# Performance work log

Hardware: AMD Instinct MI355X
Metric: run time of the kernel (lower is better)

Reference implementation:

```python
import jax, jax.numpy as jnp
import numpy as np

B, T, U, V = 4, 300, 80, 1024
DE, DD, INNER = 320, 320, 512


def setup_inputs() -> dict:
    key = jax.random.key(0)
    ks = jax.random.split(key, 6)
    enc_state = jax.random.normal(ks[0], (B, T, DE), jnp.float32)
    dec_state = jax.random.normal(ks[1], (B, U + 1, DD), jnp.float32)
    Wf = jax.random.normal(ks[2], (INNER, DE + DD), jnp.float32) / np.float32(np.sqrt(DE + DD))
    bf = jnp.zeros((INNER,), jnp.float32)
    Wp = jax.random.normal(ks[3], (V, INNER), jnp.float32) / np.float32(np.sqrt(INNER))
    bp = jnp.zeros((V,), jnp.float32)
    targets = jax.random.randint(ks[4], (B, U), 1, V).astype(jnp.int32)  # labels avoid blank=0
    inputs_length = jnp.full((B,), T, jnp.int32)
    targets_length = jnp.full((B,), U, jnp.int32)
    return {"enc_state": enc_state, "dec_state": dec_state, "Wf": Wf, "bf": bf,
            "Wp": Wp, "bp": bp, "targets": targets,
            "inputs_length": inputs_length, "targets_length": targets_length}


def joint_logits(enc, dec, Wf, bf, Wp, bp):
    # Linear over concat([enc, dec]) == Linear(enc) + Linear(dec): avoids materializing the concat.
    de = enc.shape[-1]
    Wf_e, Wf_d = Wf[:, :de], Wf[:, de:]
    enc_p = jnp.einsum('btd,id->bti', enc, Wf_e)   # [B,T,inner]
    dec_p = jnp.einsum('bud,id->bui', dec, Wf_d)   # [B,U1,inner]
    h = jnp.tanh(enc_p[:, :, None, :] + dec_p[:, None, :, :] + bf)  # [B,T,U1,inner]
    return jnp.einsum('btui,vi->btuv', h, Wp) + bp  # [B,T,U1,V]


def rnnt_loss(log_probs, targets, t_len, u_len):
    # log_probs: [B,T,U1,V], blank index 0.
    lp_blank = log_probs[..., 0]  # [B,T,U1]
    lp_emit = jnp.take_along_axis(log_probs[:, :, :-1, :], targets[:, None, :, None], axis=3)[..., 0]  # [B,T,U]
    # row0: alpha[0,u] = sum_{k<u} emit[0,k]
    row0 = jnp.pad(jnp.cumsum(lp_emit[:, 0, :], axis=-1), ((0, 0), (1, 0)))  # [B,U1]

    def outer(alpha_prev, xs):
        blank_prev, emit_cur = xs  # [B,U1], [B,U]
        first = alpha_prev[:, 0] + blank_prev[:, 0]  # [B]

        def inner(c, x):
            a_plus_b, e = x  # [B],[B]
            c2 = jnp.logaddexp(a_plus_b, c + e)
            return c2, c2
        xs_in = ((alpha_prev[:, 1:] + blank_prev[:, 1:]).T, emit_cur.T)  # [U,B]
        _, rest = jax.lax.scan(inner, first, xs_in)  # [U,B]
        row = jnp.concatenate([first[None, :], rest], axis=0).T  # [B,U1]
        return row, row

    xs = (jnp.swapaxes(lp_blank[:, :-1, :], 0, 1), jnp.swapaxes(lp_emit[:, 1:, :], 0, 1))
    _, rows = jax.lax.scan(outer, row0, xs)  # [T-1,B,U1]
    alpha = jnp.concatenate([row0[None], rows], axis=0)  # [T,B,U1]
    bidx = jnp.arange(alpha.shape[1])
    ll = alpha[t_len - 1, bidx, u_len] + lp_blank[bidx, t_len - 1, u_len]
    return -jnp.mean(ll)


def reference(enc_state, dec_state, Wf, bf, Wp, bp, targets, inputs_length, targets_length):
    logits = joint_logits(enc_state, dec_state, Wf, bf, Wp, bp).astype(jnp.float32)
    log_probs = jax.nn.log_softmax(logits, axis=-1)
    return rnnt_loss(log_probs, targets, inputs_length, targets_length)
```

## Files before the change

### kernel.cpp

```cpp
#include <hip/hip_runtime.h>

#define B_DIM 4
#define T_DIM 300
#define U_DIM 80
#define UP1   81
#define V_DIM 1024
#define NINNER 512
#define NROWS (B_DIM * T_DIM * UP1)
#define EP_ROWS (B_DIM * T_DIM)
#define DP_ROWS (B_DIM * UP1)
#define NDIAG_B 380
#define NDIAG_E 379
#define DSTRIDE 82
#define WF_PART 163840
#define LOG2E 1.44269504088896341f
#define LN2   0.69314718055994531f
#define NEGF  -1e30f

typedef float f32x4 __attribute__((ext_vector_type(4)));
typedef short short8 __attribute__((ext_vector_type(8)));
typedef short short4v __attribute__((ext_vector_type(4)));
typedef __bf16 bf16x8 __attribute__((ext_vector_type(8)));

static __device__ __forceinline__ short f2bf(float f) {
  return (short)__builtin_bit_cast(unsigned short, (__bf16)f);
}
static __device__ __forceinline__ float bf2f(short s) {
  unsigned int u = ((unsigned int)(unsigned short)s) << 16;
  return __builtin_bit_cast(float, u);
}
static __device__ __forceinline__ float tanh_fast(float x) {
  float e = __builtin_amdgcn_exp2f(x * 2.88539008177792681f);
  return 1.0f - 2.0f * __builtin_amdgcn_rcpf(e + 1.0f);
}
static __device__ __forceinline__ float lse2_2(float a, float b) {
  float mx = fmaxf(a, b), mn = fminf(a, b);
  return mx + __builtin_amdgcn_logf(1.0f + __builtin_amdgcn_exp2f(mn - mx));
}
static __device__ __forceinline__ float ror1f(float x) {
  int r = __builtin_amdgcn_update_dpp(0, __builtin_bit_cast(int, x),
                                      0x13C , 0xF, 0xF, true);
  return __builtin_bit_cast(float, r);
}
static __device__ __forceinline__ float readlanef(float x, int l) {
  return __builtin_bit_cast(float,
      __builtin_amdgcn_readlane(__builtin_bit_cast(int, x), l));
}

__global__ __launch_bounds__(256) void fill_kernel(float* __restrict__ dst, int n4) {
  int i = blockIdx.x * 256 + threadIdx.x;
  if (i < n4) ((f32x4*)dst)[i] = (f32x4){NEGF, NEGF, NEGF, NEGF};
}

__global__ __launch_bounds__(256) void cvt_kernel(
    const float* __restrict__ Wf, const float* __restrict__ Wp,
    short* __restrict__ WfB, short* __restrict__ WpB) {
  int idx = blockIdx.x * 256 + threadIdx.x;
  const int nf = (512 * 640) / 4;
  const int np = (V_DIM * NINNER) / 4;
  if (idx < nf) {
    float4 v = ((const float4*)Wf)[idx];
    int flat = idx * 4;
    int c = flat / 640;
    int kc = flat - c * 640;
    int part = (kc >= 320);
    int k0 = kc - (part ? 320 : 0);
    int dest = (part ? WF_PART : 0)
             + ((c >> 4) * 10 + (k0 >> 5)) * 512
             + (((k0 >> 3) & 3) * 16 + (c & 15)) * 8 + (k0 & 7);
    short4v o;
    o[0] = f2bf(v.x); o[1] = f2bf(v.y); o[2] = f2bf(v.z); o[3] = f2bf(v.w);
    *(short4v*)(WfB + dest) = o;
  } else if (idx < nf + np) {
    int j = idx - nf;
    float4 v = ((const float4*)Wp)[j];
    int flat = j * 4;
    int c = flat >> 9;
    int k0 = flat & 511;
    int dest = ((c >> 4) * 16 + (k0 >> 5)) * 512
             + (((k0 >> 3) & 3) * 16 + (c & 15)) * 8 + (k0 & 7);
    short4v o;
    o[0] = f2bf(v.x); o[1] = f2bf(v.y); o[2] = f2bf(v.z); o[3] = f2bf(v.w);
    *(short4v*)(WpB + dest) = o;
  }
}

#define EP_BLOCKS 19
__global__ __launch_bounds__(256) void proj_kernel(
    const float* __restrict__ enc, const float* __restrict__ dec,
    const short* __restrict__ WfB, const float* __restrict__ bfv,
    short* __restrict__ epB, short* __restrict__ dpB) {
  const int half = blockIdx.x & 1;
  const int ob = blockIdx.x >> 1;
  const bool is_dp = (ob >= EP_BLOCKS);
  const int row0 = (is_dp ? ob - EP_BLOCKS : ob) * 64;
  const int nrows = is_dp ? DP_ROWS : EP_ROWS;
  const float* __restrict__ src = is_dp ? dec : enc;
  const short* __restrict__ bb = WfB + (is_dp ? WF_PART : 0);
  short* __restrict__ out = is_dp ? dpB : epB;

  __shared__ short As[64 * 320];
  const int tid = threadIdx.x;

  #pragma unroll
  for (int it = 0; it < 10; ++it) {
    int chunk = it * 256 + tid;
    int m = chunk / 40;
    int c = chunk - m * 40;
    int r = row0 + m;
    short8 hv;
    #pragma unroll
    for (int j = 0; j < 8; ++j) hv[j] = 0;
    if (r < nrows) {
      const float* p = src + (size_t)r * 320 + c * 8;
      float4 a0 = *(const float4*)p;
      float4 a1 = *(const float4*)(p + 4);
      hv[0] = f2bf(a0.x); hv[1] = f2bf(a0.y); hv[2] = f2bf(a0.z); hv[3] = f2bf(a0.w);
      hv[4] = f2bf(a1.x); hv[5] = f2bf(a1.y); hv[6] = f2bf(a1.z); hv[7] = f2bf(a1.w);
    }
    int off = (m * 640 + c * 16) ^ ((m & 7) << 4);
    *(short8*)((char*)As + off) = hv;
  }
  __syncthreads();

  const int lane = tid & 63, wid = tid >> 6;
  const int lr = lane & 15, g = lane >> 4;

  int lin[4], xm[4];
  #pragma unroll
  for (int mf = 0; mf < 4; ++mf) {
    int row = mf * 16 + lr;
    lin[mf] = row * 640 + g * 16;
    xm[mf] = (row & 7) << 4;
  }

  const int n0 = half * 256 + wid * 64;
  const short* bptr[4];
  float bfc[4];
  #pragma unroll
  for (int nf2 = 0; nf2 < 4; ++nf2) {
    bptr[nf2] = bb + (n0 / 16 + nf2) * 5120 + lane * 8;
    bfc[nf2] = is_dp ? bfv[n0 + nf2 * 16 + lr] : 0.f;
  }
  f32x4 acc[4][4];
  #pragma unroll
  for (int mf = 0; mf < 4; ++mf)
    #pragma unroll
    for (int nf2 = 0; nf2 < 4; ++nf2)
      acc[mf][nf2] = (f32x4){0.f, 0.f, 0.f, 0.f};

  #pragma unroll 2
  for (int kk = 0; kk < 10; ++kk) {
    bf16x8 av[4], bv[4];
    #pragma unroll
    for (int mf = 0; mf < 4; ++mf) {
      int off = (lin[mf] + (kk << 6)) ^ xm[mf];
      av[mf] = __builtin_bit_cast(bf16x8, *(const short8*)((const char*)As + off));
    }
    #pragma unroll
    for (int nf2 = 0; nf2 < 4; ++nf2)
      bv[nf2] = __builtin_bit_cast(bf16x8, *(const short8*)(bptr[nf2] + kk * 512));
    #pragma unroll
    for (int mf = 0; mf < 4; ++mf)
      #pragma unroll
      for (int nf2 = 0; nf2 < 4; ++nf2)
        acc[mf][nf2] = __builtin_amdgcn_mfma_f32_16x16x32_bf16(av[mf], bv[nf2], acc[mf][nf2], 0, 0, 0);
  }
  #pragma unroll
  for (int mf = 0; mf < 4; ++mf)
    #pragma unroll
    for (int nf2 = 0; nf2 < 4; ++nf2)
      #pragma unroll
      for (int rr = 0; rr < 4; ++rr) {
        int rowl = mf * 16 + g * 4 + rr;
        int grow = row0 + rowl;
        if (grow < nrows) {
          int col = n0 + nf2 * 16 + lr;
          out[(size_t)grow * NINNER + col] = f2bf(acc[mf][nf2][rr] + bfc[nf2]);
        }
      }
}

#define JROWS 64
__global__ __launch_bounds__(512) void joint_kernel(
    const short* __restrict__ epB, const short* __restrict__ dpB,
    const short* __restrict__ WpB, const float* __restrict__ bp,
    const int* __restrict__ tgt,
    float* __restrict__ lpb_p, float* __restrict__ lpe_p) {
  extern __shared__ char hbuf[];
  __shared__ int ep_off[JROWS], dp_off[JROWS], bld_off[JROWS], eld_off[JROWS], tgt_s[JROWS];
  __shared__ float l0_s[JROWS], lt_s[JROWS];
  __shared__ float ws_s[8][JROWS];

  const int tid = threadIdx.x;
  const int row0 = blockIdx.x * JROWS;

  if (tid < JROWS) {
    int gr = row0 + tid;
    if (gr < NROWS) {
      int b = gr / (T_DIM * UP1);
      int rem = gr - b * (T_DIM * UP1);
      int t = rem / UP1;
      int u = rem - t * UP1;
      ep_off[tid] = (b * T_DIM + t) * NINNER;
      dp_off[tid] = (b * UP1 + u) * NINNER;
      bld_off[tid] = (b * NDIAG_B + (t + u)) * DSTRIDE + 1 + u;
      eld_off[tid] = (u < U_DIM) ? ((b * NDIAG_E + (t + u)) * DSTRIDE + 2 + u) : -1;
      tgt_s[tid] = (u < U_DIM) ? tgt[b * U_DIM + u] : 0;
    } else {
      ep_off[tid] = 0; dp_off[tid] = 0; bld_off[tid] = -1; eld_off[tid] = -1; tgt_s[tid] = 0;
    }
    l0_s[tid] = 0.f; lt_s[tid] = 0.f;
  }
  __syncthreads();

  #pragma unroll 2
  for (int it = 0; it < 8; ++it) {
    int chunk = it * 512 + tid;
    int m = chunk >> 6, c = chunk & 63;
    short8 hv;
    #pragma unroll
    for (int j = 0; j < 8; ++j) hv[j] = 0;
    if (bld_off[m] >= 0) {
      short8 ev = *(const short8*)(epB + ep_off[m] + c * 8);
      short8 dv = *(const short8*)(dpB + dp_off[m] + c * 8);
      #pragma unroll
      for (int j = 0; j < 8; ++j)
        hv[j] = f2bf(tanh_fast(bf2f(ev[j]) + bf2f(dv[j])));
    }
    int off = ((m << 10) + (c << 4)) ^ ((m & 7) << 4);
    *(short8*)(hbuf + off) = hv;
  }
  __syncthreads();

  const int lane = tid & 63, wid = tid >> 6;
  const int lr = lane & 15, g = lane >> 4;

  int lin[4], xm[4];
  #pragma unroll
  for (int mf = 0; mf < 4; ++mf) {
    int row = mf * 16 + lr;
    lin[mf] = (row << 10) + (g << 4);
    xm[mf] = (row & 7) << 4;
  }
  int tv[4][4];
  #pragma unroll
  for (int mf = 0; mf < 4; ++mf)
    #pragma unroll
    for (int rr = 0; rr < 4; ++rr)
      tv[mf][rr] = tgt_s[mf * 16 + g * 4 + rr];

  float rsum[4][4];
  #pragma unroll
  for (int mf = 0; mf < 4; ++mf)
    #pragma unroll
    for (int rr = 0; rr < 4; ++rr) rsum[mf][rr] = 0.f;

  #pragma unroll
  for (int sc = 0; sc < 2; ++sc) {
    const int n0 = wid * 128 + sc * 64;
    const short* bptr[4];
    float bpv[4];
    #pragma unroll
    for (int nf = 0; nf < 4; ++nf) {
      bptr[nf] = WpB + (n0 / 16 + nf) * 8192 + lane * 8;
      bpv[nf] = bp[n0 + nf * 16 + lr] * LOG2E;
    }
    f32x4 acc[4][4];
    #pragma unroll
    for (int mf = 0; mf < 4; ++mf)
      #pragma unroll
      for (int nf = 0; nf < 4; ++nf)
        acc[mf][nf] = (f32x4){0.f, 0.f, 0.f, 0.f};

    #pragma unroll 2
    for (int kk = 0; kk < 16; ++kk) {
      bf16x8 av[4], bv[4];
      #pragma unroll
      for (int mf = 0; mf < 4; ++mf) {
        int off = (lin[mf] + (kk << 6)) ^ xm[mf];
        av[mf] = __builtin_bit_cast(bf16x8, *(const short8*)(hbuf + off));
      }
      #pragma unroll
      for (int nf = 0; nf < 4; ++nf)
        bv[nf] = __builtin_bit_cast(bf16x8, *(const short8*)(bptr[nf] + kk * 512));
      __builtin_amdgcn_s_setprio(1);
      #pragma unroll
      for (int mf = 0; mf < 4; ++mf)
        #pragma unroll
        for (int nf = 0; nf < 4; ++nf)
          acc[mf][nf] = __builtin_amdgcn_mfma_f32_16x16x32_bf16(av[mf], bv[nf], acc[mf][nf], 0, 0, 0);
      __builtin_amdgcn_s_setprio(0);
    }
    #pragma unroll
    for (int mf = 0; mf < 4; ++mf)
      #pragma unroll
      for (int rr = 0; rr < 4; ++rr) {
        float x0 = __builtin_fmaf(acc[mf][0][rr], LOG2E, bpv[0]);
        float x1 = __builtin_fmaf(acc[mf][1][rr], LOG2E, bpv[1]);
        float x2 = __builtin_fmaf(acc[mf][2][rr], LOG2E, bpv[2]);
        float x3 = __builtin_fmaf(acc[mf][3][rr], LOG2E, bpv[3]);
        int rowl = mf * 16 + g * 4 + rr;
        if (wid == 0 && sc == 0 && lr == 0) l0_s[rowl] = x0;
        int dtv = tv[mf][rr] - n0;
        if (dtv >= 0 && dtv < 64 && (dtv & 15) == lr) {
          int nfi = dtv >> 4;
          lt_s[rowl] = (nfi == 0) ? x0 : (nfi == 1) ? x1 : (nfi == 2) ? x2 : x3;
        }
        rsum[mf][rr] += __builtin_amdgcn_exp2f(x0) + __builtin_amdgcn_exp2f(x1)
                      + __builtin_amdgcn_exp2f(x2) + __builtin_amdgcn_exp2f(x3);
      }
  }
  #pragma unroll
  for (int mf = 0; mf < 4; ++mf)
    #pragma unroll
    for (int rr = 0; rr < 4; ++rr) {
      float s_ = rsum[mf][rr];
      #pragma unroll
      for (int o = 1; o < 16; o <<= 1) s_ += __shfl_xor(s_, o);
      if (lr == 0) ws_s[wid][mf * 16 + g * 4 + rr] = s_;
    }
  __syncthreads();
  if (tid < JROWS) {
    int bo = bld_off[tid];
    if (bo >= 0) {
      float S = 0.f;
      #pragma unroll
      for (int w = 0; w < 8; ++w) S += ws_s[w][tid];
      float lse2v = __builtin_amdgcn_logf(S);
      lpb_p[bo] = l0_s[tid] - lse2v;
      int eo = eld_off[tid];
      if (eo >= 0) lpe_p[eo] = lt_s[tid] - lse2v;
    }
  }
}

#define ACH 8
#define NCH 48
__global__ __launch_bounds__(256) void alpha_kernel(
    const float* __restrict__ lpb_p, const float* __restrict__ lpe_p,
    const int* __restrict__ ilen, const int* __restrict__ ulen_,
    float* __restrict__ out) {
  __shared__ float lls[B_DIM];
  const int tid = threadIdx.x;
  const int b = tid >> 6;
  const int lane = tid & 63;
  const float NEG = NEGF;
  const int tl = ilen[b], ul = ulen_[b];
  const int dstar = tl - 1 + ul;

  const int u0 = lane;
  const int u1 = 64 + lane;
  const bool act1 = (u1 <= 80);
  const int uc1 = act1 ? u1 : 80;

  const float* pbb = lpb_p + (size_t)b * (NDIAG_B * DSTRIDE);
  const float* peb = lpe_p + (size_t)b * (NDIAG_E * DSTRIDE);

  float Ab0r[ACH], Ab0m[ACH], Ae0r[ACH], Ae0m[ACH];
  float Ab1r[ACH], Ab1m[ACH], Ae1r[ACH], Ae1m[ACH];
  float Bb0r[ACH], Bb0m[ACH], Be0r[ACH], Be0m[ACH];
  float Bb1r[ACH], Bb1m[ACH], Be1r[ACH], Be1m[ACH];

  #define ALOAD(P, c)                                                        \
    {                                                                        \
      _Pragma("unroll")                                                      \
      for (int j = 0; j < ACH; ++j) {                                        \
        int dd = (c) * ACH + j;                                              \
        int ddb = dd < NDIAG_B ? dd : NDIAG_B - 1;                           \
        int dde = dd < NDIAG_E ? dd : NDIAG_E - 1;                           \
        const float* rb_ = pbb + ddb * DSTRIDE + 1;                          \
        const float* re_ = peb + dde * DSTRIDE + 2;                          \
        P##b0r[j] = rb_[u0];                                                 \
        P##b0m[j] = rb_[u0 - 1];                                             \
        P##e0r[j] = re_[u0 - 1];                                             \
        P##e0m[j] = re_[u0 - 2];                                             \
        P##b1r[j] = rb_[uc1];                                                \
        P##b1m[j] = rb_[uc1 - 1];                                            \
        P##e1r[j] = re_[uc1 - 1];                                            \
        P##e1m[j] = re_[uc1 - 2];                                            \
      }                                                                      \
    }

  #define ACOMP(P, c)                                                        \
    {                                                                        \
      _Pragma("unroll")                                                      \
      for (int q = 0; q < ACH / 2; ++q) {                                    \
        const int j = 2 * q;                                                 \
        const int s1 = (c) * ACH + j + 1;                                    \
             \
        float a63 = readlanef(pa0, 63), a62 = readlanef(pa0, 62);            \
        float s0m1 = ror1f(pa0);                                             \
        float s0m2 = ror1f(s0m1);                                            \
        float s1m1r = ror1f(pa1);                                            \
        float s1m2r = ror1f(s1m1r);                                          \
        float s1m1 = (lane == 0) ? a63 : s1m1r;                              \
        float s1m2 = (lane == 0) ? a62 : ((lane == 1) ? a63 : s1m2r);        \
        float na0, na1;                                                      \
        {               \
          float b1 = P##b0r[j], b2 = P##b0r[j + 1];                          \
          float e1 = P##e0r[j], e2 = P##e0r[j + 1];                          \
          float b1m = P##b0m[j], e1m = P##e0m[j];                            \
          float T1 = b1 + b2;                                                \
          float T2 = lse2_2(e1 + b2, b1m + e2);                              \
          float T3 = e1m + e2;                                               \
          float p0 = pa0 + T1;                                               \
          float p1 = s0m1 + T2;                                              \
          float p2 = s0m2 + T3;                                              \
          float mx = fmaxf(fmaxf(p0, p1), p2);                               \
          float ss = __builtin_amdgcn_exp2f(p0 - mx)                         \
                   + __builtin_amdgcn_exp2f(p1 - mx)                         \
                   + __builtin_amdgcn_exp2f(p2 - mx);                        \
          na0 = fmaxf(mx + __builtin_amdgcn_logf(ss), NEG);                  \
        }                                                                    \
        {                                                        \
          float b1 = P##b1r[j], b2 = P##b1r[j + 1];                          \
          float e1 = P##e1r[j], e2 = P##e1r[j + 1];                          \
          float b1m = P##b1m[j], e1m = P##e1m[j];                            \
          float T1 = b1 + b2;                                                \
          float T2 = lse2_2(e1 + b2, b1m + e2);                              \
          float T3 = e1m + e2;                                               \
          float p0 = pa1 + T1;                                               \
          float p1 = s1m1 + T2;                                              \
          float p2 = s1m2 + T3;                                              \
          float mx = fmaxf(fmaxf(p0, p1), p2);                               \
          float ss = __builtin_amdgcn_exp2f(p0 - mx)                         \
                   + __builtin_amdgcn_exp2f(p1 - mx)                         \
                   + __builtin_amdgcn_exp2f(p2 - mx);                        \
          na1 = fmaxf(mx + __builtin_amdgcn_logf(ss), NEG);                  \
        }                                                                    \
        if (s1 == dstar) {   \
          float vo0 = lse2_2(pa0 + P##b0r[j], s0m1 + P##e0r[j]);             \
          if (u0 == ul) fin = vo0;                                           \
          float vo1 = lse2_2(pa1 + P##b1r[j], s1m1 + P##e1r[j]);             \
          if (act1 && u1 == ul) fin = vo1;                                   \
        }                                                                    \
        pa0 = na0; pa1 = na1;                                                \
        if (s1 + 1 == dstar) {              \
          if (u0 == ul) fin = pa0;                                           \
          if (act1 && u1 == ul) fin = pa1;                                   \
        }                                                                    \
      }                                                                      \
    }

  float pa0 = (u0 == 0) ? 0.f : NEG;
  float pa1 = NEG;
  float fin = NEG;
  if (dstar == 0 && u0 == ul) fin = pa0;

  ALOAD(A, 0);
  for (int p = 0; p < NCH / 2; ++p) {
    const int cA = 2 * p, cB = 2 * p + 1;
    ALOAD(B, cB);
    ACOMP(A, cA);
    ALOAD(A, cA + 2);
    ACOMP(B, cB);
  }

  #pragma unroll
  for (int o = 32; o; o >>= 1) fin = fmaxf(fin, __shfl_xor(fin, o));
  if (lane == 0) {
    float last = pbb[(size_t)dstar * DSTRIDE + 1 + ul];
    lls[b] = fin + last;
  }
  __syncthreads();
  if (tid == 0)
    out[0] = -(lls[0] + lls[1] + lls[2] + lls[3]) * (LN2 * 0.25f);
}

extern "C" void kernel_launch(void* const* d_in, const int* in_sizes, int n_in,
                              void* d_out, int out_size, void* d_ws, size_t ws_size,
                              hipStream_t stream) {
  const float* enc = (const float*)d_in[0];
  const float* dec = (const float*)d_in[1];
  const float* Wf  = (const float*)d_in[2];
  const float* bfv = (const float*)d_in[3];
  const float* Wp  = (const float*)d_in[4];
  const float* bp  = (const float*)d_in[5];
  const int* targets = (const int*)d_in[6];
  const int* ilen    = (const int*)d_in[7];
  const int* ulen    = (const int*)d_in[8];
  float* out = (float*)d_out;
  char* ws = (char*)d_ws;

  short* WfB   = (short*)(ws + 0);
  short* WpB   = (short*)(ws + 655360);
  short* epB   = (short*)(ws + 1703936);
  short* dpB   = (short*)(ws + 2932736);
  float* lpb_p = (float*)(ws + 3264512);
  float* lpe_p = (float*)(ws + 3763072);
  const int FILL_N4 = (4 * NDIAG_B * DSTRIDE + 4 * NDIAG_E * DSTRIDE) / 4;

  fill_kernel<<<(FILL_N4 + 255) / 256, 256, 0, stream>>>(lpb_p, FILL_N4);
  cvt_kernel<<<832, 256, 0, stream>>>(Wf, Wp, WfB, WpB);
  proj_kernel<<<50, 256, 0, stream>>>(enc, dec, WfB, bfv, epB, dpB);
  joint_kernel<<<(NROWS + JROWS - 1) / JROWS, 512, 65536, stream>>>(epB, dpB, WpB, bp, targets, lpb_p, lpe_p);
  alpha_kernel<<<1, 256, 0, stream>>>(lpb_p, lpe_p, ilen, ulen, out);
}
```

Measured before the change: 218.2 us.

## Interleave blank/emit log-probs per diagonal and fold fill into convert kernel

Blank and emit log-probs now share one diagonal-major buffer with the two values interleaved per u. The alpha recursion can then fetch the four values it needs per lane and diagonal with a single 16-byte load instead of eight scalar loads. The separate -inf fill kernel is merged into the weight conversion kernel by adding extra blocks, which saves a launch. The trade-off is unaligned vector loads in the serial alpha kernel and a larger padded buffer to fill.

After: 198.9 us. -8.9%, faster.

```diff
diff --git a/kernel.cpp b/kernel.cpp
--- a/kernel.cpp
+++ b/kernel.cpp
@@ -9,9 +9,9 @@
 #define NROWS (B_DIM * T_DIM * UP1)
 #define EP_ROWS (B_DIM * T_DIM)
 #define DP_ROWS (B_DIM * UP1)
-#define NDIAG_B 380
-#define NDIAG_E 379
-#define DSTRIDE 82
+#define NDIAG 380
+#define ZSTR  168
+#define ZROWS (B_DIM * NDIAG + 8)
 #define WF_PART 163840
 #define LOG2E 1.44269504088896341f
 #define LN2   0.69314718055994531f
@@ -46,19 +46,20 @@
   return __builtin_bit_cast(float,
       __builtin_amdgcn_readlane(__builtin_bit_cast(int, x), l));
 }
-
-__global__ __launch_bounds__(256) void fill_kernel(float* __restrict__ dst, int n4) {
-  int i = blockIdx.x * 256 + threadIdx.x;
-  if (i < n4) ((f32x4*)dst)[i] = (f32x4){NEGF, NEGF, NEGF, NEGF};
-}
-
+static __device__ __forceinline__ f32x4 load4u(const float* p) {
+  f32x4 v;
+  __builtin_memcpy(&v, p, 16);
+  return v;
+}
+
+#define CVT_NF 81920
+#define CVT_NP 131072
+#define FILL_N4 ((ZROWS * ZSTR) / 4)
 __global__ __launch_bounds__(256) void cvt_kernel(
     const float* __restrict__ Wf, const float* __restrict__ Wp,
-    short* __restrict__ WfB, short* __restrict__ WpB) {
+    short* __restrict__ WfB, short* __restrict__ WpB, float* __restrict__ Z) {
   int idx = blockIdx.x * 256 + threadIdx.x;
-  const int nf = (512 * 640) / 4;
-  const int np = (V_DIM * NINNER) / 4;
-  if (idx < nf) {
+  if (idx < CVT_NF) {
     float4 v = ((const float4*)Wf)[idx];
     int flat = idx * 4;
     int c = flat / 640;
@@ -71,8 +72,8 @@
     short4v o;
     o[0] = f2bf(v.x); o[1] = f2bf(v.y); o[2] = f2bf(v.z); o[3] = f2bf(v.w);
     *(short4v*)(WfB + dest) = o;
-  } else if (idx < nf + np) {
-    int j = idx - nf;
+  } else if (idx < CVT_NF + CVT_NP) {
+    int j = idx - CVT_NF;
     float4 v = ((const float4*)Wp)[j];
     int flat = j * 4;
     int c = flat >> 9;
@@ -82,6 +83,9 @@
     short4v o;
     o[0] = f2bf(v.x); o[1] = f2bf(v.y); o[2] = f2bf(v.z); o[3] = f2bf(v.w);
     *(short4v*)(WpB + dest) = o;
+  } else {
+    int i = idx - (CVT_NF + CVT_NP);
+    if (i < FILL_N4) ((f32x4*)Z)[i] = (f32x4){NEGF, NEGF, NEGF, NEGF};
   }
 }
 
@@ -185,8 +189,7 @@
 __global__ __launch_bounds__(512) void joint_kernel(
     const short* __restrict__ epB, const short* __restrict__ dpB,
     const short* __restrict__ WpB, const float* __restrict__ bp,
-    const int* __restrict__ tgt,
-    float* __restrict__ lpb_p, float* __restrict__ lpe_p) {
+    const int* __restrict__ tgt, float* __restrict__ Z) {
   extern __shared__ char hbuf[];
   __shared__ int ep_off[JROWS], dp_off[JROWS], bld_off[JROWS], eld_off[JROWS], tgt_s[JROWS];
   __shared__ float l0_s[JROWS], lt_s[JROWS];
@@ -204,8 +207,9 @@
       int u = rem - t * UP1;
       ep_off[tid] = (b * T_DIM + t) * NINNER;
       dp_off[tid] = (b * UP1 + u) * NINNER;
-      bld_off[tid] = (b * NDIAG_B + (t + u)) * DSTRIDE + 1 + u;
-      eld_off[tid] = (u < U_DIM) ? ((b * NDIAG_E + (t + u)) * DSTRIDE + 2 + u) : -1;
+      int zrow = (b * NDIAG + (t + u)) * ZSTR;
+      bld_off[tid] = zrow + 4 + 2 * u;
+      eld_off[tid] = (u < U_DIM) ? (zrow + 4 + 2 * u + 1) : -1;
       tgt_s[tid] = (u < U_DIM) ? tgt[b * U_DIM + u] : 0;
     } else {
       ep_off[tid] = 0; dp_off[tid] = 0; bld_off[tid] = -1; eld_off[tid] = -1; tgt_s[tid] = 0;
@@ -328,9 +332,9 @@
       #pragma unroll
       for (int w = 0; w < 8; ++w) S += ws_s[w][tid];
       float lse2v = __builtin_amdgcn_logf(S);
-      lpb_p[bo] = l0_s[tid] - lse2v;
+      Z[bo] = l0_s[tid] - lse2v;
       int eo = eld_off[tid];
-      if (eo >= 0) lpe_p[eo] = lt_s[tid] - lse2v;
+      if (eo >= 0) Z[eo] = lt_s[tid] - lse2v;
     }
   }
 }
@@ -338,7 +342,7 @@
 #define ACH 8
 #define NCH 48
 __global__ __launch_bounds__(256) void alpha_kernel(
-    const float* __restrict__ lpb_p, const float* __restrict__ lpe_p,
+    const float* __restrict__ Z,
     const int* __restrict__ ilen, const int* __restrict__ ulen_,
     float* __restrict__ out) {
   __shared__ float lls[B_DIM];
@@ -354,31 +358,18 @@
   const bool act1 = (u1 <= 80);
   const int uc1 = act1 ? u1 : 80;
 
-  const float* pbb = lpb_p + (size_t)b * (NDIAG_B * DSTRIDE);
-  const float* peb = lpe_p + (size_t)b * (NDIAG_E * DSTRIDE);
-
-  float Ab0r[ACH], Ab0m[ACH], Ae0r[ACH], Ae0m[ACH];
-  float Ab1r[ACH], Ab1m[ACH], Ae1r[ACH], Ae1m[ACH];
-  float Bb0r[ACH], Bb0m[ACH], Be0r[ACH], Be0m[ACH];
-  float Bb1r[ACH], Bb1m[ACH], Be1r[ACH], Be1m[ACH];
+  const float* Zb = Z + (size_t)b * (NDIAG * ZSTR);
+
+  f32x4 Aq0[ACH], Aq1[ACH], Bq0[ACH], Bq1[ACH];
 
   #define ALOAD(P, c)                                                        \
     {                                                                        \
+      const float* base0 = Zb + (c) * (ACH * ZSTR) + 1 + 2 * u0;             \
+      const float* base1 = Zb + (c) * (ACH * ZSTR) + 1 + 2 * uc1;            \
       _Pragma("unroll")                                                      \
       for (int j = 0; j < ACH; ++j) {                                        \
-        int dd = (c) * ACH + j;                                              \
-        int ddb = dd < NDIAG_B ? dd : NDIAG_B - 1;                           \
-        int dde = dd < NDIAG_E ? dd : NDIAG_E - 1;                           \
-        const float* rb_ = pbb + ddb * DSTRIDE + 1;                          \
-        const float* re_ = peb + dde * DSTRIDE + 2;                          \
-        P##b0r[j] = rb_[u0];                                                 \
-        P##b0m[j] = rb_[u0 - 1];                                             \
-        P##e0r[j] = re_[u0 - 1];                                             \
-        P##e0m[j] = re_[u0 - 2];                                             \
-        P##b1r[j] = rb_[uc1];                                                \
-        P##b1m[j] = rb_[uc1 - 1];                                            \
-        P##e1r[j] = re_[uc1 - 1];                                            \
-        P##e1m[j] = re_[uc1 - 2];                                            \
+        P##q0[j] = load4u(base0 + j * ZSTR);                                 \
+        P##q1[j] = load4u(base1 + j * ZSTR);                                 \
       }                                                                      \
     }
 
@@ -388,7 +379,7 @@
       for (int q = 0; q < ACH / 2; ++q) {                                    \
         const int j = 2 * q;                                                 \
         const int s1 = (c) * ACH + j + 1;                                    \
-             \
+                                    \
         float a63 = readlanef(pa0, 63), a62 = readlanef(pa0, 62);            \
         float s0m1 = ror1f(pa0);                                             \
         float s0m2 = ror1f(s0m1);                                            \
@@ -397,13 +388,11 @@
         float s1m1 = (lane == 0) ? a63 : s1m1r;                              \
         float s1m2 = (lane == 0) ? a62 : ((lane == 1) ? a63 : s1m2r);        \
         float na0, na1;                                                      \
-        {               \
-          float b1 = P##b0r[j], b2 = P##b0r[j + 1];                          \
-          float e1 = P##e0r[j], e2 = P##e0r[j + 1];                          \
-          float b1m = P##b0m[j], e1m = P##e0m[j];                            \
-          float T1 = b1 + b2;                                                \
-          float T2 = lse2_2(e1 + b2, b1m + e2);                              \
-          float T3 = e1m + e2;                                               \
+        {                        \
+          f32x4 v = P##q0[j], w = P##q0[j + 1];                              \
+          float T1 = v[3] + w[3];                                            \
+          float T2 = lse2_2(v[2] + w[3], v[1] + w[2]);                       \
+          float T3 = v[0] + w[2];                                            \
           float p0 = pa0 + T1;                                               \
           float p1 = s0m1 + T2;                                              \
           float p2 = s0m2 + T3;                                              \
@@ -414,12 +403,10 @@
           na0 = fmaxf(mx + __builtin_amdgcn_logf(ss), NEG);                  \
         }                                                                    \
         {                                                        \
-          float b1 = P##b1r[j], b2 = P##b1r[j + 1];                          \
-          float e1 = P##e1r[j], e2 = P##e1r[j + 1];                          \
-          float b1m = P##b1m[j], e1m = P##e1m[j];                            \
-          float T1 = b1 + b2;                                                \
-          float T2 = lse2_2(e1 + b2, b1m + e2);                              \
-          float T3 = e1m + e2;                                               \
+          f32x4 v = P##q1[j], w = P##q1[j + 1];                              \
+          float T1 = v[3] + w[3];                                            \
+          float T2 = lse2_2(v[2] + w[3], v[1] + w[2]);                       \
+          float T3 = v[0] + w[2];                                            \
           float p0 = pa1 + T1;                                               \
           float p1 = s1m1 + T2;                                              \
           float p2 = s1m2 + T3;                                              \
@@ -429,10 +416,10 @@
                    + __builtin_amdgcn_exp2f(p2 - mx);                        \
           na1 = fmaxf(mx + __builtin_amdgcn_logf(ss), NEG);                  \
         }                                                                    \
-        if (s1 == dstar) {   \
-          float vo0 = lse2_2(pa0 + P##b0r[j], s0m1 + P##e0r[j]);             \
+        if (s1 == dstar) {                   \
+          float vo0 = lse2_2(pa0 + P##q0[j][3], s0m1 + P##q0[j][2]);         \
           if (u0 == ul) fin = vo0;                                           \
-          float vo1 = lse2_2(pa1 + P##b1r[j], s1m1 + P##e1r[j]);             \
+          float vo1 = lse2_2(pa1 + P##q1[j][3], s1m1 + P##q1[j][2]);         \
           if (act1 && u1 == ul) fin = vo1;                                   \
         }                                                                    \
         pa0 = na0; pa1 = na1;                                                \
@@ -460,7 +447,7 @@
   #pragma unroll
   for (int o = 32; o; o >>= 1) fin = fmaxf(fin, __shfl_xor(fin, o));
   if (lane == 0) {
-    float last = pbb[(size_t)dstar * DSTRIDE + 1 + ul];
+    float last = Zb[(size_t)dstar * ZSTR + 4 + 2 * ul];
     lls[b] = fin + last;
   }
   __syncthreads();
@@ -483,17 +470,14 @@
   float* out = (float*)d_out;
   char* ws = (char*)d_ws;
 
-  short* WfB   = (short*)(ws + 0);
-  short* WpB   = (short*)(ws + 655360);
-  short* epB   = (short*)(ws + 1703936);
-  short* dpB   = (short*)(ws + 2932736);
-  float* lpb_p = (float*)(ws + 3264512);
-  float* lpe_p = (float*)(ws + 3763072);
-  const int FILL_N4 = (4 * NDIAG_B * DSTRIDE + 4 * NDIAG_E * DSTRIDE) / 4;
-
-  fill_kernel<<<(FILL_N4 + 255) / 256, 256, 0, stream>>>(lpb_p, FILL_N4);
-  cvt_kernel<<<832, 256, 0, stream>>>(Wf, Wp, WfB, WpB);
+  short* WfB = (short*)(ws + 0);
+  short* WpB = (short*)(ws + 655360);
+  short* epB = (short*)(ws + 1703936);
+  short* dpB = (short*)(ws + 2932736);
+  float* Z   = (float*)(ws + 3264512);
+
+  cvt_kernel<<<1083, 256, 0, stream>>>(Wf, Wp, WfB, WpB, Z);
   proj_kernel<<<50, 256, 0, stream>>>(enc, dec, WfB, bfv, epB, dpB);
-  joint_kernel<<<(NROWS + JROWS - 1) / JROWS, 512, 65536, stream>>>(epB, dpB, WpB, bp, targets, lpb_p, lpe_p);
-  alpha_kernel<<<1, 256, 0, stream>>>(lpb_p, lpe_p, ilen, ulen, out);
-}
+  joint_kernel<<<(NROWS + JROWS - 1) / JROWS, 512, 65536, stream>>>(epB, dpB, WpB, bp, targets, Z);
+  alpha_kernel<<<1, 256, 0, stream>>>(Z, ilen, ulen, out);
+}
```
